# Performance work log

Hardware: AMD Instinct MI355X
Metric: run time of the kernel (lower is better)

Reference implementation:

```python
import jax, jax.numpy as jnp
import numpy as np

N_EMBD = 1024
N_HEAD = 16
HEAD_DIM = N_EMBD // N_HEAD


def setup_inputs() -> dict:
    key = jax.random.key(0)
    kx, kqkv, kw, kb = jax.random.split(key, 4)
    B, T = 4, 2048
    x = jax.random.normal(kx, (B, T, N_EMBD), dtype=jnp.float32)
    # nn.Linear weights stored [out, in]; apply as x @ W.T
    w_qkv = jax.random.normal(kqkv, (3 * N_EMBD, N_EMBD), dtype=jnp.float32) * (N_EMBD ** -0.5)
    w_out = jax.random.normal(kw, (N_EMBD, N_EMBD), dtype=jnp.float32) * (N_EMBD ** -0.5)
    b_out = jax.random.normal(kb, (N_EMBD,), dtype=jnp.float32) * 0.01
    return {"x": x, "w_qkv": w_qkv, "w_out": w_out, "b_out": b_out}


def reference(x, w_qkv, w_out, b_out):
    B, T, C = x.shape
    H, D = N_HEAD, HEAD_DIM
    qkv = jnp.einsum('btc,fc->btf', x, w_qkv)  # [B,T,3C]
    q, k, v = jnp.split(qkv, 3, axis=-1)
    q = q.reshape(B, T, H, D).transpose(0, 2, 1, 3)  # [B,H,T,D]
    k = k.reshape(B, T, H, D).transpose(0, 2, 1, 3)
    v = v.reshape(B, T, H, D).transpose(0, 2, 1, 3)
    att = jnp.einsum('bhqd,bhkd->bhqk', q, k) * (D ** -0.5)  # [B,H,T,T]
    causal = jnp.tril(jnp.ones((T, T), dtype=bool))
    att = jnp.where(causal[None, None], att, jnp.float32(-jnp.inf))
    att = jax.nn.softmax(att, axis=-1)
    out = jnp.einsum('bhqk,bhkd->bhqd', att, v)  # [B,H,T,D]
    out = out.transpose(0, 2, 1, 3).reshape(B, T, C)
    return jnp.einsum('btc,oc->bto', out, w_out) + b_out
```

## Files before the change

### kernel.cpp

```cpp
#include <hip/hip_runtime.h>
#include <stdint.h>

#define SEQ 2048
#define C3 3072
#define C1 1024

typedef __bf16 bf16x8 __attribute__((ext_vector_type(8)));
typedef short short8 __attribute__((ext_vector_type(8)));
typedef float f32x4 __attribute__((ext_vector_type(4)));
typedef float f32x16 __attribute__((ext_vector_type(16)));
typedef const __attribute__((address_space(1))) void gv_t;
typedef __attribute__((address_space(3))) void lv_t;

#if __has_builtin(__builtin_amdgcn_exp2f)
#define EXP2(x) __builtin_amdgcn_exp2f(x)
#else
#define EXP2(x) exp2f(x)
#endif

static __device__ __forceinline__ unsigned short f2bf(float f) {
  union { float ff; unsigned u; } x; x.ff = f;
  unsigned u = x.u + 0x7FFFu + ((x.u >> 16) & 1u);
  return (unsigned short)(u >> 16);
}
static __device__ __forceinline__ unsigned rne2(float lo, float hi) {
  return (unsigned)f2bf(lo) | ((unsigned)f2bf(hi) << 16);
}
static __device__ __forceinline__ unsigned pk2(float lo, float hi) {
  union { float f; unsigned u; } a, b; a.f = lo; b.f = hi;
  return __builtin_amdgcn_perm(b.u, a.u, 0x07060302);
}

__global__ void k_cvt(const float* __restrict__ in, unsigned short* __restrict__ out, int n4) {
  int i = blockIdx.x * 256 + threadIdx.x;
  if (i >= n4) return;
  f32x4 v = ((const f32x4*)in)[i];
  ushort4 o;
  o.x = f2bf(v[0]); o.y = f2bf(v[1]); o.z = f2bf(v[2]); o.w = f2bf(v[3]);
  ((ushort4*)out)[i] = o;
}

template<int MODE>
__global__ __launch_bounds__(256, 2) void k_gemm(
    const unsigned short* __restrict__ A, const unsigned short* __restrict__ B,
    void* __restrict__ Cout, const float* __restrict__ bias, int M, int N, int K)
{
  __shared__ unsigned short As[128 * 64];
  __shared__ unsigned short Bs[128 * 64];
  const int tid = threadIdx.x;
  const int w = tid >> 6, l = tid & 63;
  const int lane15 = l & 15, quad = l >> 4;
  const int m0 = blockIdx.y * 128, n0 = blockIdx.x * 128;
  const int wm = (w >> 1) * 64, wn = (w & 1) * 64;

  f32x4 acc[4][4];
#pragma unroll
  for (int i = 0; i < 4; i++)
#pragma unroll
    for (int j = 0; j < 4; j++) acc[i][j] = (f32x4){0.f, 0.f, 0.f, 0.f};

  const int srow = l >> 3;
  const int g_off = ((l & 7) ^ (srow & 7)) * 8;
  const unsigned short* Ab = A + (size_t)(m0 + w * 32 + srow) * K + g_off;
  const unsigned short* Bb = B + (size_t)(n0 + w * 32 + srow) * K + g_off;
  const int rsl = lane15 & 7;

  for (int k0 = 0; k0 < K; k0 += 64) {
    __syncthreads();
#pragma unroll
    for (int i = 0; i < 4; i++) {
      int rb = w * 32 + i * 8;
      __builtin_amdgcn_global_load_lds((gv_t*)(Ab + (size_t)(i * 8) * K + k0),
                                       (lv_t*)&As[rb * 64], 16, 0, 0);
      __builtin_amdgcn_global_load_lds((gv_t*)(Bb + (size_t)(i * 8) * K + k0),
                                       (lv_t*)&Bs[rb * 64], 16, 0, 0);
    }
    __syncthreads();
#pragma unroll
    for (int s = 0; s < 2; s++) {
      bf16x8 af[4], bfr[4];
      const int slot = ((s * 4 + quad) ^ rsl) * 8;
#pragma unroll
      for (int t = 0; t < 4; t++) {
        af[t]  = *(const bf16x8*)&As[(wm + t * 16 + lane15) * 64 + slot];
        bfr[t] = *(const bf16x8*)&Bs[(wn + t * 16 + lane15) * 64 + slot];
      }
#pragma unroll
      for (int i = 0; i < 4; i++)
#pragma unroll
        for (int j = 0; j < 4; j++)
          acc[i][j] = __builtin_amdgcn_mfma_f32_16x16x32_bf16(af[i], bfr[j], acc[i][j], 0, 0, 0);
    }
  }

  if (MODE == 0) {
    unsigned short* Cp = (unsigned short*)Cout;
#pragma unroll
    for (int i = 0; i < 4; i++) {
      int rowb = m0 + wm + i * 16 + quad * 4;
#pragma unroll
      for (int j = 0; j < 4; j++) {
        int col = n0 + wn + j * 16 + lane15;
        float s = (col < 1024) ? 0.18033688f : 1.0f;
#pragma unroll
        for (int r = 0; r < 4; r++)
          Cp[(size_t)(rowb + r) * N + col] = f2bf(acc[i][j][r] * s);
      }
    }
  } else {
    float* Cp = (float*)Cout;
#pragma unroll
    for (int i = 0; i < 4; i++) {
      int rowb = m0 + wm + i * 16 + quad * 4;
#pragma unroll
      for (int j = 0; j < 4; j++) {
        int col = n0 + wn + j * 16 + lane15;
        float bv = bias[col];
#pragma unroll
        for (int r = 0; r < 4; r++)
          Cp[(size_t)(rowb + r) * N + col] = acc[i][j][r] + bv;
      }
    }
  }
}

__global__ void k_vt(const unsigned short* __restrict__ qkv, unsigned short* __restrict__ vT) {
  __shared__ unsigned short T[64 * 65];
  int t = threadIdx.x;
  int bh = blockIdx.y, b = bh >> 4, h = bh & 15;
  int t0 = blockIdx.x * 64;
  int tokl = t >> 2, dl = (t & 3) * 16;
  const unsigned short* g = qkv + (size_t)(b * SEQ + t0 + tokl) * C3 + 2 * C1 + h * 64 + dl;
  short8 v0 = *(const short8*)g;
  short8 v1 = *(const short8*)(g + 8);
#pragma unroll
  for (int j = 0; j < 8; j++) {
    T[(dl + j) * 65 + tokl]     = (unsigned short)v0[j];
    T[(dl + 8 + j) * 65 + tokl] = (unsigned short)v1[j];
  }
  __syncthreads();
  int d2 = t >> 2, tk = (t & 3) * 16;
  union { unsigned short s[16]; short8 v[2]; } o;
#pragma unroll
  for (int j = 0; j < 16; j++) o.s[j] = T[d2 * 65 + tk + j];
  unsigned short* og = vT + ((size_t)bh * 64 + d2) * SEQ + t0 + tk;
  *(short8*)og = o.v[0];
  *(short8*)(og + 8) = o.v[1];
}

__global__ __launch_bounds__(256, 3) void k_attn(
    const unsigned short* __restrict__ qkv, const unsigned short* __restrict__ vT,
    unsigned short* __restrict__ att)
{
  __shared__ unsigned short buf[16384];
  const int tid = threadIdx.x;
  const int w = tid >> 6, l = tid & 63;
  const int l31 = l & 31, hl = l >> 5;
  const int bh = blockIdx.x, b = bh >> 4, h = bh & 15;
  const int qt = (int)(gridDim.y - 1 - blockIdx.y);
  const int q0 = qt * 128;
  const int nkt = qt + 1;
  const size_t tokb = (size_t)b * SEQ;
  const int qmy = q0 + w * 32 + l31;

  bf16x8 qf[4];
  {
    const unsigned short* qp = qkv + (tokb + q0 + w * 32 + l31) * C3 + h * 64 + hl * 8;
#pragma unroll
    for (int ks = 0; ks < 4; ks++) qf[ks] = *(const bf16x8*)(qp + ks * 16);
  }

  f32x16 O[2];
#pragma unroll
  for (int i = 0; i < 16; i++) { O[0][i] = 0.f; O[1][i] = 0.f; }
  float mrun = -1e30f, lrun = 0.f;

  const int krow_l = l >> 3, kslot = l & 7;
  const int vrow_l = l >> 4, vslot = l & 15;
  unsigned short* Kb = &buf[0];
  unsigned short* Vb = &buf[8192];

  for (int kt = 0; kt < nkt; kt++) {
    const int k0 = kt << 7;
    __syncthreads();
    {
#pragma unroll
      for (int i = 0; i < 4; i++) {
        int rb = (w * 4 + i) * 8;
        int row = rb + krow_l;
        int ck = kslot ^ (row & 7);
        const unsigned short* g = qkv + (tokb + k0 + row) * C3 + C1 + h * 64 + ck * 8;
        __builtin_amdgcn_global_load_lds((gv_t*)g, (lv_t*)&Kb[rb * 64], 16, 0, 0);
      }
#pragma unroll
      for (int i = 0; i < 4; i++) {
        int rb = (w * 4 + i) * 4;
        int row = rb + vrow_l;
        int ck = vslot ^ (row & 15);
        const unsigned short* g = vT + ((size_t)bh * 64 + row) * SEQ + k0 + ck * 8;
        __builtin_amdgcn_global_load_lds((gv_t*)g, (lv_t*)&Vb[rb * 128], 16, 0, 0);
      }
    }
    __syncthreads();

    const bool diag = (kt == nkt - 1);

#pragma unroll
    for (int ht = 0; ht < 2; ht++) {
      if (diag && (ht * 2 > w)) continue;
      const bool two = !diag || (ht * 2 + 1 <= w);

      f32x16 stL[2];
#pragma unroll
      for (int lm = 0; lm < 2; lm++) {
        if (lm == 1 && !two) continue;
#pragma unroll
        for (int i = 0; i < 16; i++) stL[lm][i] = 0.f;
        int row = (ht * 2 + lm) * 32 + l31;
        const unsigned short* kr = &Kb[row * 64];
#pragma unroll
        for (int ks = 0; ks < 4; ks++) {
          bf16x8 a = *(const bf16x8*)&kr[((((ks << 1) | hl)) ^ (row & 7)) * 8];
          stL[lm] = __builtin_amdgcn_mfma_f32_32x32x16_bf16(a, qf[ks], stL[lm], 0, 0, 0);
        }
      }

      if (diag) {
#pragma unroll
        for (int lm = 0; lm < 2; lm++) {
          if (ht * 2 + lm == w) {
#pragma unroll
            for (int r = 0; r < 16; r++) {
              int key = k0 + w * 32 + (r & 3) + ((r >> 2) << 3) + (hl << 2);
              if (key > qmy) stL[lm][r] = -1e30f;
            }
          }
        }
      }

      float vmax = -1e30f;
#pragma unroll
      for (int lm = 0; lm < 2; lm++) {
        if (lm == 1 && !two) continue;
#pragma unroll
        for (int r = 0; r < 16; r++) vmax = fmaxf(vmax, stL[lm][r]);
      }
      vmax = fmaxf(vmax, __shfl_xor(vmax, 32, 64));
      float mnew = fmaxf(mrun, vmax);
      float alpha = EXP2(mrun - mnew);

      float psum = 0.f;
      unsigned pk[2][8];
#pragma unroll
      for (int lm = 0; lm < 2; lm++) {
        if (lm == 1 && !two) continue;
#pragma unroll
        for (int r = 0; r < 16; r++) {
          float pv = EXP2(stL[lm][r] - mnew);
          stL[lm][r] = pv;
          psum += pv;
        }
#pragma unroll
        for (int k2 = 0; k2 < 8; k2++)
          pk[lm][k2] = pk2(stL[lm][2 * k2], stL[lm][2 * k2 + 1]);
      }
      psum += __shfl_xor(psum, 32, 64);
      lrun = lrun * alpha + psum;
      mrun = mnew;

#pragma unroll
      for (int i = 0; i < 16; i++) { O[0][i] *= alpha; O[1][i] *= alpha; }

#pragma unroll
      for (int ks4 = 0; ks4 < 4; ks4++) {
        int lm = ks4 >> 1, e = ks4 & 1;
        if (lm == 1 && !two) continue;
        unsigned pA0 = pk[lm][4 * e], pA1 = pk[lm][4 * e + 1];
        unsigned pB0 = pk[lm][4 * e + 2], pB1 = pk[lm][4 * e + 3];
        unsigned w0 = hl ? pA0 : pB0, w1 = hl ? pA1 : pB1;
        unsigned r0 = (unsigned)__shfl_xor((int)w0, 32, 64);
        unsigned r1 = (unsigned)__shfl_xor((int)w1, 32, 64);
        unsigned s0 = hl ? pB0 : pA0, s1 = hl ? pB1 : pA1;
        union { unsigned u[4]; bf16x8 v; } Bf;
        Bf.u[0] = hl ? r0 : s0; Bf.u[1] = hl ? r1 : s1;
        Bf.u[2] = hl ? s0 : r0; Bf.u[3] = hl ? s1 : r1;
        int kk = ht * 4 + ks4;
#pragma unroll
        for (int dt = 0; dt < 2; dt++) {
          int row = dt * 32 + l31;
          bf16x8 a = *(const bf16x8*)&Vb[row * 128 + (((2 * kk + hl)) ^ (row & 15)) * 8];
          O[dt] = __builtin_amdgcn_mfma_f32_32x32x16_bf16(a, Bf.v, O[dt], 0, 0, 0);
        }
      }
    }
  }

  __syncthreads();
  float linv = __builtin_amdgcn_rcpf(lrun);
  unsigned* epi32 = (unsigned*)&buf[0];
  const int base = w * 2304 + l31 * 72;
#pragma unroll
  for (int dt = 0; dt < 2; dt++)
#pragma unroll
    for (int c = 0; c < 4; c++) {
      int d0 = dt * 32 + c * 8 + hl * 4;
      epi32[(base + d0) >> 1]     = rne2(O[dt][4 * c] * linv, O[dt][4 * c + 1] * linv);
      epi32[(base + d0 + 2) >> 1] = rne2(O[dt][4 * c + 2] * linv, O[dt][4 * c + 3] * linv);
    }
  __builtin_amdgcn_s_waitcnt(0);
  {
    int q = l >> 1, hf = l & 1;
    const unsigned short* ep = &buf[w * 2304 + q * 72 + hf * 32];
    unsigned short* og = att + (tokb + q0 + w * 32 + q) * C1 + h * 64 + hf * 32;
#pragma unroll
    for (int c2 = 0; c2 < 4; c2++)
      *(bf16x8*)(og + c2 * 8) = *(const bf16x8*)&ep[c2 * 8];
  }
}

extern "C" void kernel_launch(void* const* d_in, const int* in_sizes, int n_in,
                              void* d_out, int out_size, void* d_ws, size_t ws_size,
                              hipStream_t stream) {
  const float* x     = (const float*)d_in[0];
  const float* w_qkv = (const float*)d_in[1];
  const float* w_out = (const float*)d_in[2];
  const float* b_out = (const float*)d_in[3];
  float* out = (float*)d_out;

  unsigned short* xb  = (unsigned short*)d_ws;
  unsigned short* wqb = xb  + (size_t)8192 * 1024;
  unsigned short* wob = wqb + (size_t)3072 * 1024;
  unsigned short* qkv = wob + (size_t)1024 * 1024;
  unsigned short* att = qkv + (size_t)8192 * 3072;
  unsigned short* vT  = att + (size_t)8192 * 1024;

  k_cvt<<<8192, 256, 0, stream>>>(x, xb, 8192 * 1024 / 4);
  k_cvt<<<3072, 256, 0, stream>>>(w_qkv, wqb, 3072 * 1024 / 4);
  k_cvt<<<1024, 256, 0, stream>>>(w_out, wob, 1024 * 1024 / 4);
  k_gemm<0><<<dim3(24, 64), 256, 0, stream>>>(xb, wqb, (void*)qkv, nullptr, 8192, 3072, 1024);
  k_vt<<<dim3(32, 64), 256, 0, stream>>>(qkv, vT);
  k_attn<<<dim3(64, 16), 256, 0, stream>>>(qkv, vT, att);
  k_gemm<1><<<dim3(8, 64), 256, 0, stream>>>(att, wob, (void*)out, b_out, 8192, 1024, 1024);
}
```

Baseline: 231.7 us.

## Fuse V transpose into QKV GEMM epilogue and pair causal q-tiles per block

The QKV GEMM epilogue now writes the V columns straight into the transposed vT layout, which removes the separate k_vt kernel and its extra round trip through global memory. The attention kernel now gives each block a pair of query tiles (pr, 15-pr), so every block does the same amount of causal work. Both tiles share each K/V tile load, which halves K/V traffic for the shorter tile. In exchange, register use roughly doubles (two Q and O sets), LDS grows for a separate epilogue area, and occupancy drops from 3 to 2 blocks per CU. The vT stores in the GEMM are also strided 8-byte writes, which may coalesce poorly.

After: 240.7 us. 3.9% more time.

```diff
diff --git a/kernel.cpp b/kernel.cpp
--- a/kernel.cpp
+++ b/kernel.cpp
@@ -43,7 +43,8 @@
 template<int MODE>
 __global__ __launch_bounds__(256, 2) void k_gemm(
     const unsigned short* __restrict__ A, const unsigned short* __restrict__ B,
-    void* __restrict__ Cout, const float* __restrict__ bias, int M, int N, int K)
+    void* __restrict__ Cout, const float* __restrict__ bias,
+    unsigned short* __restrict__ vTout, int M, int N, int K)
 {
   __shared__ unsigned short As[128 * 64];
   __shared__ unsigned short Bs[128 * 64];
@@ -94,17 +95,33 @@
   }
 
   if (MODE == 0) {
-    unsigned short* Cp = (unsigned short*)Cout;
-#pragma unroll
-    for (int i = 0; i < 4; i++) {
-      int rowb = m0 + wm + i * 16 + quad * 4;
-#pragma unroll
-      for (int j = 0; j < 4; j++) {
-        int col = n0 + wn + j * 16 + lane15;
-        float s = (col < 1024) ? 0.18033688f : 1.0f;
-#pragma unroll
-        for (int r = 0; r < 4; r++)
-          Cp[(size_t)(rowb + r) * N + col] = f2bf(acc[i][j][r] * s);
+    if (n0 >= 2048) {
+#pragma unroll
+      for (int i = 0; i < 4; i++) {
+        int rowb = m0 + wm + i * 16 + quad * 4;
+        int bb = rowb >> 11, t = rowb & 2047;
+#pragma unroll
+        for (int j = 0; j < 4; j++) {
+          int hd = n0 + wn + j * 16 + lane15 - 2048;
+          unsigned short* vp = vTout +
+              ((size_t)((bb << 4) + (hd >> 6)) * 64 + (hd & 63)) * SEQ + t;
+          *(uint2*)vp = make_uint2(rne2(acc[i][j][0], acc[i][j][1]),
+                                   rne2(acc[i][j][2], acc[i][j][3]));
+        }
+      }
+    } else {
+      unsigned short* Cp = (unsigned short*)Cout;
+      const float s = (n0 < 1024) ? 0.18033688f : 1.0f;
+#pragma unroll
+      for (int i = 0; i < 4; i++) {
+        int rowb = m0 + wm + i * 16 + quad * 4;
+#pragma unroll
+        for (int j = 0; j < 4; j++) {
+          int col = n0 + wn + j * 16 + lane15;
+#pragma unroll
+          for (int r = 0; r < 4; r++)
+            Cp[(size_t)(rowb + r) * N + col] = f2bf(acc[i][j][r] * s);
+        }
       }
     }
   } else {
@@ -124,87 +141,44 @@
   }
 }
 
-__global__ void k_vt(const unsigned short* __restrict__ qkv, unsigned short* __restrict__ vT) {
-  __shared__ unsigned short T[64 * 65];
-  int t = threadIdx.x;
-  int bh = blockIdx.y, b = bh >> 4, h = bh & 15;
-  int t0 = blockIdx.x * 64;
-  int tokl = t >> 2, dl = (t & 3) * 16;
-  const unsigned short* g = qkv + (size_t)(b * SEQ + t0 + tokl) * C3 + 2 * C1 + h * 64 + dl;
-  short8 v0 = *(const short8*)g;
-  short8 v1 = *(const short8*)(g + 8);
-#pragma unroll
-  for (int j = 0; j < 8; j++) {
-    T[(dl + j) * 65 + tokl]     = (unsigned short)v0[j];
-    T[(dl + 8 + j) * 65 + tokl] = (unsigned short)v1[j];
-  }
-  __syncthreads();
-  int d2 = t >> 2, tk = (t & 3) * 16;
-  union { unsigned short s[16]; short8 v[2]; } o;
-#pragma unroll
-  for (int j = 0; j < 16; j++) o.s[j] = T[d2 * 65 + tk + j];
-  unsigned short* og = vT + ((size_t)bh * 64 + d2) * SEQ + t0 + tk;
-  *(short8*)og = o.v[0];
-  *(short8*)(og + 8) = o.v[1];
-}
-
-__global__ __launch_bounds__(256, 3) void k_attn(
+__global__ __launch_bounds__(256, 2) void k_attn(
     const unsigned short* __restrict__ qkv, const unsigned short* __restrict__ vT,
     unsigned short* __restrict__ att)
 {
-  __shared__ unsigned short buf[16384];
+  __shared__ unsigned short buf[25600];
   const int tid = threadIdx.x;
   const int w = tid >> 6, l = tid & 63;
   const int l31 = l & 31, hl = l >> 5;
   const int bh = blockIdx.x, b = bh >> 4, h = bh & 15;
-  const int qt = (int)(gridDim.y - 1 - blockIdx.y);
-  const int q0 = qt * 128;
-  const int nkt = qt + 1;
+  const int pr = blockIdx.y;
+  const int qtA = pr, qtB = 15 - pr;
   const size_t tokb = (size_t)b * SEQ;
-  const int qmy = q0 + w * 32 + l31;
-
-  bf16x8 qf[4];
+  const int q0A = qtA << 7, q0B = qtB << 7;
+  const int qmyA = q0A + w * 32 + l31, qmyB = q0B + w * 32 + l31;
+
+  bf16x8 qfA[4], qfB[4];
   {
-    const unsigned short* qp = qkv + (tokb + q0 + w * 32 + l31) * C3 + h * 64 + hl * 8;
-#pragma unroll
-    for (int ks = 0; ks < 4; ks++) qf[ks] = *(const bf16x8*)(qp + ks * 16);
+    const unsigned short* qpA = qkv + (tokb + q0A + w * 32 + l31) * C3 + h * 64 + hl * 8;
+    const unsigned short* qpB = qkv + (tokb + q0B + w * 32 + l31) * C3 + h * 64 + hl * 8;
+#pragma unroll
+    for (int ks = 0; ks < 4; ks++) {
+      qfA[ks] = *(const bf16x8*)(qpA + ks * 16);
+      qfB[ks] = *(const bf16x8*)(qpB + ks * 16);
+    }
   }
 
-  f32x16 O[2];
-#pragma unroll
-  for (int i = 0; i < 16; i++) { O[0][i] = 0.f; O[1][i] = 0.f; }
-  float mrun = -1e30f, lrun = 0.f;
+  f32x16 OA[2], OB[2];
+#pragma unroll
+  for (int i = 0; i < 16; i++) { OA[0][i] = 0.f; OA[1][i] = 0.f; OB[0][i] = 0.f; OB[1][i] = 0.f; }
+  float mA = -1e30f, lA = 0.f, mB = -1e30f, lB = 0.f;
 
   const int krow_l = l >> 3, kslot = l & 7;
   const int vrow_l = l >> 4, vslot = l & 15;
   unsigned short* Kb = &buf[0];
   unsigned short* Vb = &buf[8192];
 
-  for (int kt = 0; kt < nkt; kt++) {
-    const int k0 = kt << 7;
-    __syncthreads();
-    {
-#pragma unroll
-      for (int i = 0; i < 4; i++) {
-        int rb = (w * 4 + i) * 8;
-        int row = rb + krow_l;
-        int ck = kslot ^ (row & 7);
-        const unsigned short* g = qkv + (tokb + k0 + row) * C3 + C1 + h * 64 + ck * 8;
-        __builtin_amdgcn_global_load_lds((gv_t*)g, (lv_t*)&Kb[rb * 64], 16, 0, 0);
-      }
-#pragma unroll
-      for (int i = 0; i < 4; i++) {
-        int rb = (w * 4 + i) * 4;
-        int row = rb + vrow_l;
-        int ck = vslot ^ (row & 15);
-        const unsigned short* g = vT + ((size_t)bh * 64 + row) * SEQ + k0 + ck * 8;
-        __builtin_amdgcn_global_load_lds((gv_t*)g, (lv_t*)&Vb[rb * 128], 16, 0, 0);
-      }
-    }
-    __syncthreads();
-
-    const bool diag = (kt == nkt - 1);
-
+  auto tile_update = [&](f32x16* O, float& mrun, float& lrun, const bf16x8* qf,
+                         int qmy, int k0, bool diag) {
 #pragma unroll
     for (int ht = 0; ht < 2; ht++) {
       if (diag && (ht * 2 > w)) continue;
@@ -293,29 +267,58 @@
         }
       }
     }
-  }
-
-  __syncthreads();
-  float linv = __builtin_amdgcn_rcpf(lrun);
-  unsigned* epi32 = (unsigned*)&buf[0];
-  const int base = w * 2304 + l31 * 72;
-#pragma unroll
-  for (int dt = 0; dt < 2; dt++)
-#pragma unroll
-    for (int c = 0; c < 4; c++) {
-      int d0 = dt * 32 + c * 8 + hl * 4;
-      epi32[(base + d0) >> 1]     = rne2(O[dt][4 * c] * linv, O[dt][4 * c + 1] * linv);
-      epi32[(base + d0 + 2) >> 1] = rne2(O[dt][4 * c + 2] * linv, O[dt][4 * c + 3] * linv);
-    }
-  __builtin_amdgcn_s_waitcnt(0);
-  {
+  };
+
+  auto epilogue = [&](const f32x16* O, float lrun, int q0) {
+    float linv = __builtin_amdgcn_rcpf(lrun);
+    unsigned* epi32 = (unsigned*)&buf[16384];
+    const int base = w * 2304 + l31 * 72;
+#pragma unroll
+    for (int dt = 0; dt < 2; dt++)
+#pragma unroll
+      for (int c = 0; c < 4; c++) {
+        int d0 = dt * 32 + c * 8 + hl * 4;
+        epi32[(base + d0) >> 1]     = rne2(O[dt][4 * c] * linv, O[dt][4 * c + 1] * linv);
+        epi32[(base + d0 + 2) >> 1] = rne2(O[dt][4 * c + 2] * linv, O[dt][4 * c + 3] * linv);
+      }
+    __builtin_amdgcn_s_waitcnt(0);
     int q = l >> 1, hf = l & 1;
-    const unsigned short* ep = &buf[w * 2304 + q * 72 + hf * 32];
+    const unsigned short* ep = &buf[16384 + w * 2304 + q * 72 + hf * 32];
     unsigned short* og = att + (tokb + q0 + w * 32 + q) * C1 + h * 64 + hf * 32;
 #pragma unroll
     for (int c2 = 0; c2 < 4; c2++)
       *(bf16x8*)(og + c2 * 8) = *(const bf16x8*)&ep[c2 * 8];
+  };
+
+  const int nkt = qtB + 1;
+  for (int kt = 0; kt < nkt; kt++) {
+    const int k0 = kt << 7;
+    __syncthreads();
+#pragma unroll
+    for (int i = 0; i < 4; i++) {
+      int rb = (w * 4 + i) * 8;
+      int row = rb + krow_l;
+      int ck = kslot ^ (row & 7);
+      const unsigned short* g = qkv + (tokb + k0 + row) * C3 + C1 + h * 64 + ck * 8;
+      __builtin_amdgcn_global_load_lds((gv_t*)g, (lv_t*)&Kb[rb * 64], 16, 0, 0);
+    }
+#pragma unroll
+    for (int i = 0; i < 4; i++) {
+      int rb = (w * 4 + i) * 4;
+      int row = rb + vrow_l;
+      int ck = vslot ^ (row & 15);
+      const unsigned short* g = vT + ((size_t)bh * 64 + row) * SEQ + k0 + ck * 8;
+      __builtin_amdgcn_global_load_lds((gv_t*)g, (lv_t*)&Vb[rb * 128], 16, 0, 0);
+    }
+    __syncthreads();
+
+    tile_update(OB, mB, lB, qfB, qmyB, k0, kt == qtB);
+    if (kt <= qtA) {
+      tile_update(OA, mA, lA, qfA, qmyA, k0, kt == qtA);
+      if (kt == qtA) epilogue(OA, lA, q0A);
+    }
   }
+  epilogue(OB, lB, q0B);
 }
 
 extern "C" void kernel_launch(void* const* d_in, const int* in_sizes, int n_in,
@@ -337,8 +340,7 @@
   k_cvt<<<8192, 256, 0, stream>>>(x, xb, 8192 * 1024 / 4);
   k_cvt<<<3072, 256, 0, stream>>>(w_qkv, wqb, 3072 * 1024 / 4);
   k_cvt<<<1024, 256, 0, stream>>>(w_out, wob, 1024 * 1024 / 4);
-  k_gemm<0><<<dim3(24, 64), 256, 0, stream>>>(xb, wqb, (void*)qkv, nullptr, 8192, 3072, 1024);
-  k_vt<<<dim3(32, 64), 256, 0, stream>>>(qkv, vT);
-  k_attn<<<dim3(64, 16), 256, 0, stream>>>(qkv, vT, att);
-  k_gemm<1><<<dim3(8, 64), 256, 0, stream>>>(att, wob, (void*)out, b_out, 8192, 1024, 1024);
-}
+  k_gemm<0><<<dim3(24, 64), 256, 0, stream>>>(xb, wqb, (void*)qkv, nullptr, vT, 8192, 3072, 1024);
+  k_attn<<<dim3(64, 8), 256, 0, stream>>>(qkv, vT, att);
+  k_gemm<1><<<dim3(8, 64), 256, 0, stream>>>(att, wob, (void*)out, b_out, nullptr, 8192, 1024, 1024);
+}
```
